# Kernel tuning notes

Hardware: AMD Instinct MI355X
Metric: run time of the kernel (lower is better)

## Reference

```python
import jax, jax.numpy as jnp
import numpy as np

MEM_SIZE = 2000
FEA_DIM = 256
FMAP = 32
BATCH = 32
SHRINK = 0.0025
EPS = 1e-12


def setup_inputs() -> dict:
    key = jax.random.key(0)
    k1, k2, k3, k4 = jax.random.split(key, 4)
    stdv = 1.0 / np.sqrt(FEA_DIM)
    inp = {
        "input": jax.random.normal(k1, (BATCH, FEA_DIM, FMAP, FMAP), dtype=jnp.float32),
        "label_batch": jax.random.randint(k2, (BATCH,), 0, 2),
        "weight": jax.random.uniform(k3, (MEM_SIZE, FEA_DIM), dtype=jnp.float32, minval=-stdv, maxval=stdv),
        "pos_embedding": jax.random.normal(k4, (1, FEA_DIM, FMAP, FMAP), dtype=jnp.float32),
    }
    return inp


def _forward(x, weight, pos_embedding):
    b, c, h, w = x.shape
    m = weight.shape[0]
    x = x + pos_embedding  # pos=True
    xr = x.transpose(0, 2, 3, 1).reshape(-1, c)  # [b*h*w, c]
    # addressing: linear -> softmax over memory slots
    att = jax.nn.softmax(jnp.einsum('nc,mc->nm', xr, weight), axis=1)  # [N, m]
    # compact loss: MSE to nearest memory item (argmax of att before shrink)
    idx = jnp.argmax(att, axis=1)
    pos_item = weight[idx]  # [N, c]
    compact_loss = jnp.mean((xr - pos_item) ** 2)
    # distance loss: hinge on pairwise squared distances between memory items
    sq = jnp.sum(weight * weight, axis=1)
    d2 = sq[:, None] + sq[None, :] - 2.0 * (weight @ weight.T)  # [m, m]
    dist = 1.0 - d2
    dist = dist * (dist > 0).astype(dist.dtype)
    dist = jnp.triu(dist, k=1)
    distance_loss = dist.sum() * 2.0 / (m * (m - 1))
    # hard shrink relu + L1 normalize (shrink_thres > 0)
    att = jax.nn.relu(att - SHRINK) * att / (jnp.abs(att - SHRINK) + EPS)
    att = att / jnp.maximum(jnp.sum(jnp.abs(att), axis=1, keepdims=True), EPS)
    # memory read
    out = jnp.einsum('nm,mc->nc', att, weight)
    out = out.reshape(b, h, w, c).transpose(0, 3, 1, 2)
    return out, compact_loss, distance_loss


def reference(input, label_batch, weight, pos_embedding):
    return _forward(input, weight, pos_embedding)
```

## Files before the change

### kernel.cpp

```cpp
#include <hip/hip_runtime.h>
#include <hip/hip_bf16.h>

typedef unsigned char u8;
typedef unsigned short u16;
typedef unsigned int u32;
typedef long long s64;
typedef float f32x4 __attribute__((ext_vector_type(4)));
typedef long long s64x2 __attribute__((ext_vector_type(2)));

#define MEM    2000
#define FEA    256
#define SLSTR  2064
#define OSTR   265
#define XRS    264
#define POOLSZ 66048
#define OUTN   8388608
#define LSC    0.015625f

__device__ __forceinline__ u32 f2e4m3(float x) {
    float ax = fabsf(x);
    u32 s = (__builtin_bit_cast(u32, x) >> 24) & 0x80u;
    if (ax >= 448.f) return s | 0x7e;
    if (ax < 0.015625f) {
        int q = (int)rintf(ax * 512.f);
        return s | (u32)q;
    }
    int e = (int)(__builtin_bit_cast(u32, ax) >> 23) - 127;
    float scale = __builtin_bit_cast(float, (u32)((127 - e + 3) << 23));
    int q = (int)rintf(ax * scale);
    int E = e + 7;
    if (q == 16) { q = 8; E += 1; if (E > 15) return s | 0x7e; }
    return s | (u32)(E << 3) | (u32)(q & 7);
}
__device__ __forceinline__ u32 f2e4m3_fast(float v) {
    u32 u = __builtin_bit_cast(u32, v);
    u += 0x0007FFFFu + ((u >> 20) & 1u);
    int bb = (int)(u >> 20) - 0x3C0;
    return bb < 0 ? 0u : (u32)bb;
}

__global__ __launch_bounds__(256) void prep_kernel(const float* __restrict__ W,
                                                   u8* __restrict__ WTc,
                                                   u8* __restrict__ Wc,
                                                   float* __restrict__ sqv,
                                                   float* __restrict__ loss) {
    const int blk = blockIdx.x, t = threadIdx.x;
    const int m0 = blk * 8;
    {
        const int sl = t >> 5, cl = t & 31;
        const int slot = m0 + sl;
        const int ch0 = cl * 8;
        const float* wr = W + slot * 256 + ch0;
        f32x4 v0 = *(const f32x4*)wr;
        f32x4 v1 = *(const f32x4*)(wr + 4);
        float ss = v0[0]*v0[0] + v0[1]*v0[1] + v0[2]*v0[2] + v0[3]*v0[3]
                 + v1[0]*v1[0] + v1[1]*v1[1] + v1[2]*v1[2] + v1[3]*v1[3];
        ss += __shfl_xor(ss, 1); ss += __shfl_xor(ss, 2); ss += __shfl_xor(ss, 4);
        ss += __shfl_xor(ss, 8); ss += __shfl_xor(ss, 16);
        if (cl == 0) sqv[slot] = ss;
        const int c = slot >> 6, s = slot & 63;
        const int kk = cl >> 2, agp = cl & 3;
        const int kp = kk >> 1, klo = kk & 1;
        u32 lo = 0, hi = 0;
#pragma unroll
        for (int i = 0; i < 4; ++i) {
            lo |= f2e4m3(v0[i] * 16.f) << (i * 8);
            hi |= f2e4m3(v1[i] * 16.f) << (i * 8);
        }
        u8* dst = Wc + c * 16384 + (size_t)((kp * 4 + agp) * 64 + s) * 16 + klo * 8;
        *(u32*)dst = lo;
        *(u32*)(dst + 4) = hi;
    }
    {
        const int ch = t;
        const int chunk = m0 >> 6;
        const int kl0 = m0 & 63;
        const int klo = kl0 >> 5, agp = (kl0 & 31) >> 3;
        u32 lo = 0, hi = 0;
#pragma unroll
        for (int i = 0; i < 8; ++i) {
            u32 bb = f2e4m3(W[(m0 + i) * 256 + ch] * 16.f);
            if (i < 4) lo |= bb << (i * 8); else hi |= bb << ((i - 4) * 8);
        }
        u8* dst = WTc + chunk * 16384 + ch * 64 + agp * 16 + klo * 8;
        *(u32*)dst = lo;
        *(u32*)(dst + 4) = hi;
    }
    if (blk == 0 && t == 0) {
        loss[0] = 0.0f;
        loss[1] = -2000.0f / (2000.0f * 1999.0f);
    }
}

__global__ __attribute__((amdgpu_flat_work_group_size(512, 512), amdgpu_waves_per_eu(4, 4)))
void main_kernel(
        const float* __restrict__ inp, const float* __restrict__ posb,
        const u8* __restrict__ Wc, const u8* __restrict__ WTc,
        const float* __restrict__ sqv, float* __restrict__ out,
        float* __restrict__ loss) {
    __shared__ __align__(16) u8 pool[POOLSZ];
    __shared__ float sPM[4][32];
    __shared__ int   sPI[4][32];
    __shared__ float sPZ[4][32];
    __shared__ float sPD[4][32];
    __shared__ float sSS[8][32];
    __shared__ float sMax[32];
    __shared__ float sThr[32];
    __shared__ float sInv[32];

    const int t = threadIdx.x;
    const int w = t >> 6, lane = t & 63;
    const int ar = lane & 15, ag = lane >> 4;
    const int blk = blockIdx.x, b = blk >> 5, hw0 = (blk & 31) << 5;
    const int prot = ((blk >> 3) & 15) * 2;
    const int q = w & 3, rt = w >> 2;
    const int row_a = rt * 16 + ar;

    {
        const int hw = t & 31, cg = t >> 5;
        const float* ip = inp + (size_t)b * 262144 + hw0 + hw;
        const float* pp = posb + hw0 + hw;
        float ss = 0.f;
        u8* xrow = pool + hw * XRS + cg * 16;
#pragma unroll
        for (int j = 0; j < 8; ++j) {
            const int ch = cg * 16 + 2 * j;
            float v0 = ip[ch * 1024] + pp[ch * 1024];
            float v1 = ip[(ch + 1) * 1024] + pp[(ch + 1) * 1024];
            ss += v0 * v0 + v1 * v1;
            u16 pk2 = (u16)(f2e4m3(v0 * 4.f) | (f2e4m3(v1 * 4.f) << 8));
            *(u16*)(xrow + 2 * j) = pk2;
        }
        ss += __shfl_xor(ss, 32);
        if (lane < 32) sSS[w][lane] = ss;
    }
    __syncthreads();

    s64 xB[8];
#pragma unroll
    for (int kk = 0; kk < 8; ++kk)
        xB[kk] = *(const s64*)(pool + row_a * XRS + kk * 32 + ag * 8);

    const u8* wbase = Wc + ag * 1024 + (q * 16 + ar) * 16;
    const int c31 = (31 - prot) & 31;

    {
        float bm = -3e38f, zz = 0.f;
        int bi = 0x7fffffff;
#pragma unroll 4
        for (int c = 0; c < 32; ++c) {
            const int pc = (c + prot) & 31;
            const u8* p = wbase + pc * 16384;
            s64x2 w0 = *(const s64x2*)(p);
            s64x2 w1 = *(const s64x2*)(p + 4096);
            s64x2 w2 = *(const s64x2*)(p + 8192);
            s64x2 w3 = *(const s64x2*)(p + 12288);
            f32x4 a = {0.f, 0.f, 0.f, 0.f};
            a = __builtin_amdgcn_mfma_f32_16x16x32_fp8_fp8(w0[0], xB[0], a, 0, 0, 0);
            a = __builtin_amdgcn_mfma_f32_16x16x32_fp8_fp8(w0[1], xB[1], a, 0, 0, 0);
            a = __builtin_amdgcn_mfma_f32_16x16x32_fp8_fp8(w1[0], xB[2], a, 0, 0, 0);
            a = __builtin_amdgcn_mfma_f32_16x16x32_fp8_fp8(w1[1], xB[3], a, 0, 0, 0);
            a = __builtin_amdgcn_mfma_f32_16x16x32_fp8_fp8(w2[0], xB[4], a, 0, 0, 0);
            a = __builtin_amdgcn_mfma_f32_16x16x32_fp8_fp8(w2[1], xB[5], a, 0, 0, 0);
            a = __builtin_amdgcn_mfma_f32_16x16x32_fp8_fp8(w3[0], xB[6], a, 0, 0, 0);
            a = __builtin_amdgcn_mfma_f32_16x16x32_fp8_fp8(w3[1], xB[7], a, 0, 0, 0);
            if (c == c31 && q != 0) { a[0] = -3e38f; a[1] = -3e38f; a[2] = -3e38f; a[3] = -3e38f; }
            const int cb = (pc << 6) + q * 16 + ag * 4;
            const float ob = bm;
#pragma unroll
            for (int e = 0; e < 4; ++e) {
                float v = a[e]; int id = cb + e;
                bool g = (v > bm) || (v == bm && id < bi);
                bm = g ? v : bm;
                bi = g ? id : bi;
            }
            zz *= __expf((ob - bm) * LSC);
            zz += __expf((a[0] - bm) * LSC) + __expf((a[1] - bm) * LSC)
                + __expf((a[2] - bm) * LSC) + __expf((a[3] - bm) * LSC);
        }
#pragma unroll
        for (int d = 16; d < 64; d <<= 1) {
            float om = __shfl_xor(bm, d);
            int   oi = __shfl_xor(bi, d);
            float oz = __shfl_xor(zz, d);
            bool g = (om > bm) || (om == bm && oi < bi);
            float nm = g ? om : bm;
            zz = zz * __expf((bm - nm) * LSC) + oz * __expf((om - nm) * LSC);
            bm = nm;
            bi = g ? oi : bi;
        }
        if (lane < 16) {
            sPM[q][rt * 16 + lane] = bm;
            sPI[q][rt * 16 + lane] = bi;
            sPZ[q][rt * 16 + lane] = zz;
        }
    }
    __syncthreads();

    if (t < 32) {
        float M = sPM[0][t]; int I = sPI[0][t];
#pragma unroll
        for (int qq = 1; qq < 4; ++qq) {
            float m2 = sPM[qq][t]; int i2 = sPI[qq][t];
            bool g = (m2 > M) || (m2 == M && i2 < I);
            M = g ? m2 : M; I = g ? i2 : I;
        }
        float Z = 0.f;
#pragma unroll
        for (int qq = 0; qq < 4; ++qq) Z += sPZ[qq][t] * __expf((sPM[qq][t] - M) * LSC);
        sMax[t] = M;
        sThr[t] = 0.0025f * Z;
        float ssq = 0.f;
#pragma unroll
        for (int ww = 0; ww < 8; ++ww) ssq += sSS[ww][t];
        float term = ssq - 2.f * (M * LSC) + sqv[I];
#pragma unroll
        for (int d = 1; d < 32; d <<= 1) term += __shfl_xor(term, d);
        if (t == 0) atomicAdd(loss, term * (1.0f / 8388608.0f));
    }
    __syncthreads();

    {
        const float M = sMax[row_a];
        const float thrv = sThr[row_a];
        const int newoff = (((q * 2 + (ag >> 1)) & 3) << 4) | ((q >> 1) << 3) | ((ag & 1) << 2);
        const int rowbase = row_a * SLSTR + newoff;
        float den = 0.f;
#pragma unroll 4
        for (int c = 0; c < 32; ++c) {
            const int pc = (c + prot) & 31;
            const u8* p = wbase + pc * 16384;
            s64x2 w0 = *(const s64x2*)(p);
            s64x2 w1 = *(const s64x2*)(p + 4096);
            s64x2 w2 = *(const s64x2*)(p + 8192);
            s64x2 w3 = *(const s64x2*)(p + 12288);
            f32x4 a = {0.f, 0.f, 0.f, 0.f};
            a = __builtin_amdgcn_mfma_f32_16x16x32_fp8_fp8(w0[0], xB[0], a, 0, 0, 0);
            a = __builtin_amdgcn_mfma_f32_16x16x32_fp8_fp8(w0[1], xB[1], a, 0, 0, 0);
            a = __builtin_amdgcn_mfma_f32_16x16x32_fp8_fp8(w1[0], xB[2], a, 0, 0, 0);
            a = __builtin_amdgcn_mfma_f32_16x16x32_fp8_fp8(w1[1], xB[3], a, 0, 0, 0);
            a = __builtin_amdgcn_mfma_f32_16x16x32_fp8_fp8(w2[0], xB[4], a, 0, 0, 0);
            a = __builtin_amdgcn_mfma_f32_16x16x32_fp8_fp8(w2[1], xB[5], a, 0, 0, 0);
            a = __builtin_amdgcn_mfma_f32_16x16x32_fp8_fp8(w3[0], xB[6], a, 0, 0, 0);
            a = __builtin_amdgcn_mfma_f32_16x16x32_fp8_fp8(w3[1], xB[7], a, 0, 0, 0);
            if (c == c31 && q != 0) { a[0] = -3e38f; a[1] = -3e38f; a[2] = -3e38f; a[3] = -3e38f; }
            float a0 = __expf((a[0] - M) * LSC);
            float a1 = __expf((a[1] - M) * LSC);
            float a2 = __expf((a[2] - M) * LSC);
            float a3 = __expf((a[3] - M) * LSC);
            bool k0 = a0 > thrv, k1 = a1 > thrv, k2 = a2 > thrv, k3 = a3 > thrv;
            den += (k0 ? a0 : 0.f) + (k1 ? a1 : 0.f) + (k2 ? a2 : 0.f) + (k3 ? a3 : 0.f);
            u32 pk = (k0 ? f2e4m3_fast(a0 * 64.f) : 0u)
                   | ((k1 ? f2e4m3_fast(a1 * 64.f) : 0u) << 8)
                   | ((k2 ? f2e4m3_fast(a2 * 64.f) : 0u) << 16)
                   | ((k3 ? f2e4m3_fast(a3 * 64.f) : 0u) << 24);
            *(u32*)(pool + rowbase + (pc << 6)) = pk;
        }
        den += __shfl_xor(den, 16);
        den += __shfl_xor(den, 32);
        if (lane < 16) sPD[q][rt * 16 + lane] = den;
    }
    __syncthreads();
    if (t < 32) {
        float dd = sPD[0][t] + sPD[1][t] + sPD[2][t] + sPD[3][t];
        sInv[t] = dd > 0.f ? 1.0f / (1024.0f * dd) : 0.0f;
    }
    __syncthreads();

    const int ch0 = (w * 2) * 16 + ar;
    const int ch1 = ch0 + 16;
    const u8* sLr0 = pool + ar * SLSTR + ag * 16;
    const u8* sLr1 = pool + (16 + ar) * SLSTR + ag * 16;
    const u8* wt0 = WTc + ch0 * 64 + ag * 16;
    const u8* wt1 = WTc + ch1 * 64 + ag * 16;
    f32x4 o00 = {0.f,0.f,0.f,0.f}, o01 = {0.f,0.f,0.f,0.f};
    f32x4 o10 = {0.f,0.f,0.f,0.f}, o11 = {0.f,0.f,0.f,0.f};
#pragma unroll 4
    for (int c = 0; c < 32; ++c) {
        const int pc = (c + prot) & 31;
        const int cc64 = pc << 6;
        s64x2 B0 = *(const s64x2*)(wt0 + pc * 16384);
        s64x2 B1 = *(const s64x2*)(wt1 + pc * 16384);
        s64x2 A0 = *(const s64x2*)(sLr0 + cc64);
        s64x2 A1 = *(const s64x2*)(sLr1 + cc64);
        o00 = __builtin_amdgcn_mfma_f32_16x16x32_fp8_fp8(A0[0], B0[0], o00, 0, 0, 0);
        o00 = __builtin_amdgcn_mfma_f32_16x16x32_fp8_fp8(A0[1], B0[1], o00, 0, 0, 0);
        o01 = __builtin_amdgcn_mfma_f32_16x16x32_fp8_fp8(A1[0], B0[0], o01, 0, 0, 0);
        o01 = __builtin_amdgcn_mfma_f32_16x16x32_fp8_fp8(A1[1], B0[1], o01, 0, 0, 0);
        o10 = __builtin_amdgcn_mfma_f32_16x16x32_fp8_fp8(A0[0], B1[0], o10, 0, 0, 0);
        o10 = __builtin_amdgcn_mfma_f32_16x16x32_fp8_fp8(A0[1], B1[1], o10, 0, 0, 0);
        o11 = __builtin_amdgcn_mfma_f32_16x16x32_fp8_fp8(A1[0], B1[0], o11, 0, 0, 0);
        o11 = __builtin_amdgcn_mfma_f32_16x16x32_fp8_fp8(A1[1], B1[1], o11, 0, 0, 0);
    }
    __syncthreads();

    {
        float* sO = (float*)pool;
#pragma unroll
        for (int i = 0; i < 4; ++i) {
            int r0 = ag * 4 + i, r1 = 16 + ag * 4 + i;
            sO[r0 * OSTR + ch0] = o00[i] * sInv[r0];
            sO[r1 * OSTR + ch0] = o01[i] * sInv[r1];
            sO[r0 * OSTR + ch1] = o10[i] * sInv[r0];
            sO[r1 * OSTR + ch1] = o11[i] * sInv[r1];
        }
    }
    __syncthreads();
    {
        const float* sO = (const float*)pool;
        const int hw = t & 31, cq = t >> 5;
        float* op = out + (size_t)b * 262144 + hw0 + hw;
#pragma unroll
        for (int i = 0; i < 16; ++i) {
            int ch = cq + (i << 4);
            op[ch * 1024] = sO[hw * OSTR + ch];
        }
    }
}

__global__ __launch_bounds__(256) void dist_kernel(const u8* __restrict__ Wc,
                                                   const float* __restrict__ sqv,
                                                   float* __restrict__ dl) {
    __shared__ float red[4];
    int t = threadIdx.x, w = t >> 6, lane = t & 63;
    int ar = lane & 15, ag = lane >> 4;
    const int i0 = blockIdx.x << 4;
    const int ci = i0 >> 6, si0 = i0 & 63;
    s64x2 af2[4];
#pragma unroll
    for (int kp = 0; kp < 4; ++kp)
        af2[kp] = *(const s64x2*)(Wc + ci * 16384 + (size_t)((kp * 4 + ag) * 64 + si0 + ar) * 16);
    float sqi[4];
#pragma unroll
    for (int e = 0; e < 4; ++e) sqi[e] = sqv[i0 + ag * 4 + e];
    float sum = 0.f;
    for (int jt = w; jt < 125; jt += 4) {
        const int j0 = jt << 4;
        const int cj = j0 >> 6, sj0 = j0 & 63;
        f32x4 acc = {0.f, 0.f, 0.f, 0.f};
#pragma unroll
        for (int kp = 0; kp < 4; ++kp) {
            s64x2 bf = *(const s64x2*)(Wc + cj * 16384 + (size_t)((kp * 4 + ag) * 64 + sj0 + ar) * 16);
            acc = __builtin_amdgcn_mfma_f32_16x16x32_fp8_fp8(af2[kp][0], bf[0], acc, 0, 0, 0);
            acc = __builtin_amdgcn_mfma_f32_16x16x32_fp8_fp8(af2[kp][1], bf[1], acc, 0, 0, 0);
        }
        float sqj = sqv[j0 + ar];
#pragma unroll
        for (int e = 0; e < 4; ++e) {
            float dist = 1.0f - (sqi[e] + sqj - acc[e] * 0.0078125f);
            sum += dist > 0.f ? dist : 0.f;
        }
    }
#pragma unroll
    for (int d = 1; d < 64; d <<= 1) sum += __shfl_xor(sum, d);
    if (lane == 0) red[w] = sum;
    __syncthreads();
    if (t == 0) {
        float s = red[0] + red[1] + red[2] + red[3];
        atomicAdd(dl, s * (1.0f / (2000.0f * 1999.0f)));
    }
}

extern "C" void kernel_launch(void* const* d_in, const int* in_sizes, int n_in,
                              void* d_out, int out_size, void* d_ws, size_t ws_size,
                              hipStream_t stream) {
    (void)in_sizes; (void)n_in; (void)out_size; (void)ws_size;
    const float* inp  = (const float*)d_in[0];
    const float* W    = (const float*)d_in[2];
    const float* posb = (const float*)d_in[3];
    float* out = (float*)d_out;

    u8* WTc = (u8*)d_ws;
    u8* Wc  = (u8*)d_ws + 524288;
    float* sqv = (float*)((u8*)d_ws + 1048576);

    hipLaunchKernelGGL(prep_kernel, dim3(250), dim3(256), 0, stream, W, WTc, Wc, sqv, out + OUTN);
    hipLaunchKernelGGL(main_kernel, dim3(1024), dim3(512), 0, stream, inp, posb, Wc, WTc, sqv, out, out + OUTN);
    hipLaunchKernelGGL(dist_kernel, dim3(125), dim3(256), 0, stream, Wc, sqv, out + OUTN + 1);
}
```

Before: 148.2 us.

## Drop online max rescaling in softmax, use unshifted exp2 and hardware fp8 packing

The first pass now sums exp2 of the unshifted scaled logits, which removes the running-max rescale exps and their merges in the shuffle and cross-wave reductions. The second pass thresholds the unshifted exponentials and folds the max shift into a per-row scale and the final normalizer. It also replaces the software fp8 conversion with v_cvt_pk_fp8_f32 and removes the per-block chunk rotation. This cuts transcendental and integer work per element, but risks overflow because logits are not shifted before exponentiation, and dropping the rotation may increase L2 contention on the shared weight chunks.

```diff
diff --git a/kernel.cpp b/kernel.cpp
--- a/kernel.cpp
+++ b/kernel.cpp
@@ -15,7 +15,7 @@
 #define XRS    264
 #define POOLSZ 66048
 #define OUTN   8388608
-#define LSC    0.015625f
+#define LSC2   0.022542108517490387f
 
 __device__ __forceinline__ u32 f2e4m3(float x) {
     float ax = fabsf(x);
@@ -31,12 +31,6 @@
     int E = e + 7;
     if (q == 16) { q = 8; E += 1; if (E > 15) return s | 0x7e; }
     return s | (u32)(E << 3) | (u32)(q & 7);
-}
-__device__ __forceinline__ u32 f2e4m3_fast(float v) {
-    u32 u = __builtin_bit_cast(u32, v);
-    u += 0x0007FFFFu + ((u >> 20) & 1u);
-    int bb = (int)(u >> 20) - 0x3C0;
-    return bb < 0 ? 0u : (u32)bb;
 }
 
 __global__ __launch_bounds__(256) void prep_kernel(const float* __restrict__ W,
@@ -106,13 +100,13 @@
     __shared__ float sSS[8][32];
     __shared__ float sMax[32];
     __shared__ float sThr[32];
+    __shared__ float sSrw[32];
     __shared__ float sInv[32];
 
     const int t = threadIdx.x;
     const int w = t >> 6, lane = t & 63;
     const int ar = lane & 15, ag = lane >> 4;
     const int blk = blockIdx.x, b = blk >> 5, hw0 = (blk & 31) << 5;
-    const int prot = ((blk >> 3) & 15) * 2;
     const int q = w & 3, rt = w >> 2;
     const int row_a = rt * 16 + ar;
 
@@ -142,15 +136,13 @@
         xB[kk] = *(const s64*)(pool + row_a * XRS + kk * 32 + ag * 8);
 
     const u8* wbase = Wc + ag * 1024 + (q * 16 + ar) * 16;
-    const int c31 = (31 - prot) & 31;
-
-    {
-        float bm = -3e38f, zz = 0.f;
+
+    {
+        float bm = -3e38f, z0 = 0.f;
         int bi = 0x7fffffff;
 #pragma unroll 4
         for (int c = 0; c < 32; ++c) {
-            const int pc = (c + prot) & 31;
-            const u8* p = wbase + pc * 16384;
+            const u8* p = wbase + c * 16384;
             s64x2 w0 = *(const s64x2*)(p);
             s64x2 w1 = *(const s64x2*)(p + 4096);
             s64x2 w2 = *(const s64x2*)(p + 8192);
@@ -164,9 +156,8 @@
             a = __builtin_amdgcn_mfma_f32_16x16x32_fp8_fp8(w2[1], xB[5], a, 0, 0, 0);
             a = __builtin_amdgcn_mfma_f32_16x16x32_fp8_fp8(w3[0], xB[6], a, 0, 0, 0);
             a = __builtin_amdgcn_mfma_f32_16x16x32_fp8_fp8(w3[1], xB[7], a, 0, 0, 0);
-            if (c == c31 && q != 0) { a[0] = -3e38f; a[1] = -3e38f; a[2] = -3e38f; a[3] = -3e38f; }
-            const int cb = (pc << 6) + q * 16 + ag * 4;
-            const float ob = bm;
+            if (c == 31 && q != 0) { a[0] = -3e38f; a[1] = -3e38f; a[2] = -3e38f; a[3] = -3e38f; }
+            const int cb = (c << 6) + q * 16 + ag * 4;
 #pragma unroll
             for (int e = 0; e < 4; ++e) {
                 float v = a[e]; int id = cb + e;
@@ -174,25 +165,23 @@
                 bm = g ? v : bm;
                 bi = g ? id : bi;
             }
-            zz *= __expf((ob - bm) * LSC);
-            zz += __expf((a[0] - bm) * LSC) + __expf((a[1] - bm) * LSC)
-                + __expf((a[2] - bm) * LSC) + __expf((a[3] - bm) * LSC);
+            z0 += exp2f(a[0] * LSC2) + exp2f(a[1] * LSC2)
+                + exp2f(a[2] * LSC2) + exp2f(a[3] * LSC2);
         }
 #pragma unroll
         for (int d = 16; d < 64; d <<= 1) {
             float om = __shfl_xor(bm, d);
             int   oi = __shfl_xor(bi, d);
-            float oz = __shfl_xor(zz, d);
+            float oz = __shfl_xor(z0, d);
             bool g = (om > bm) || (om == bm && oi < bi);
-            float nm = g ? om : bm;
-            zz = zz * __expf((bm - nm) * LSC) + oz * __expf((om - nm) * LSC);
-            bm = nm;
+            bm = g ? om : bm;
             bi = g ? oi : bi;
+            z0 += oz;
         }
         if (lane < 16) {
             sPM[q][rt * 16 + lane] = bm;
             sPI[q][rt * 16 + lane] = bi;
-            sPZ[q][rt * 16 + lane] = zz;
+            sPZ[q][rt * 16 + lane] = z0;
         }
     }
     __syncthreads();
@@ -205,15 +194,14 @@
             bool g = (m2 > M) || (m2 == M && i2 < I);
             M = g ? m2 : M; I = g ? i2 : I;
         }
-        float Z = 0.f;
-#pragma unroll
-        for (int qq = 0; qq < 4; ++qq) Z += sPZ[qq][t] * __expf((sPM[qq][t] - M) * LSC);
+        float z0t = sPZ[0][t] + sPZ[1][t] + sPZ[2][t] + sPZ[3][t];
         sMax[t] = M;
-        sThr[t] = 0.0025f * Z;
+        sThr[t] = 0.0025f * z0t;
+        sSrw[t] = 64.f * exp2f(-M * LSC2);
         float ssq = 0.f;
 #pragma unroll
         for (int ww = 0; ww < 8; ++ww) ssq += sSS[ww][t];
-        float term = ssq - 2.f * (M * LSC) + sqv[I];
+        float term = ssq - 2.f * (M * (1.0f / 64.0f)) + sqv[I];
 #pragma unroll
         for (int d = 1; d < 32; d <<= 1) term += __shfl_xor(term, d);
         if (t == 0) atomicAdd(loss, term * (1.0f / 8388608.0f));
@@ -221,15 +209,14 @@
     __syncthreads();
 
     {
-        const float M = sMax[row_a];
-        const float thrv = sThr[row_a];
+        const float thr0 = sThr[row_a];
+        const float Srw  = sSrw[row_a];
         const int newoff = (((q * 2 + (ag >> 1)) & 3) << 4) | ((q >> 1) << 3) | ((ag & 1) << 2);
         const int rowbase = row_a * SLSTR + newoff;
-        float den = 0.f;
+        float denS = 0.f;
 #pragma unroll 4
         for (int c = 0; c < 32; ++c) {
-            const int pc = (c + prot) & 31;
-            const u8* p = wbase + pc * 16384;
+            const u8* p = wbase + c * 16384;
             s64x2 w0 = *(const s64x2*)(p);
             s64x2 w1 = *(const s64x2*)(p + 4096);
             s64x2 w2 = *(const s64x2*)(p + 8192);
@@ -243,27 +230,30 @@
             a = __builtin_amdgcn_mfma_f32_16x16x32_fp8_fp8(w2[1], xB[5], a, 0, 0, 0);
             a = __builtin_amdgcn_mfma_f32_16x16x32_fp8_fp8(w3[0], xB[6], a, 0, 0, 0);
             a = __builtin_amdgcn_mfma_f32_16x16x32_fp8_fp8(w3[1], xB[7], a, 0, 0, 0);
-            if (c == c31 && q != 0) { a[0] = -3e38f; a[1] = -3e38f; a[2] = -3e38f; a[3] = -3e38f; }
-            float a0 = __expf((a[0] - M) * LSC);
-            float a1 = __expf((a[1] - M) * LSC);
-            float a2 = __expf((a[2] - M) * LSC);
-            float a3 = __expf((a[3] - M) * LSC);
-            bool k0 = a0 > thrv, k1 = a1 > thrv, k2 = a2 > thrv, k3 = a3 > thrv;
-            den += (k0 ? a0 : 0.f) + (k1 ? a1 : 0.f) + (k2 ? a2 : 0.f) + (k3 ? a3 : 0.f);
-            u32 pk = (k0 ? f2e4m3_fast(a0 * 64.f) : 0u)
-                   | ((k1 ? f2e4m3_fast(a1 * 64.f) : 0u) << 8)
-                   | ((k2 ? f2e4m3_fast(a2 * 64.f) : 0u) << 16)
-                   | ((k3 ? f2e4m3_fast(a3 * 64.f) : 0u) << 24);
-            *(u32*)(pool + rowbase + (pc << 6)) = pk;
-        }
-        den += __shfl_xor(den, 16);
-        den += __shfl_xor(den, 32);
-        if (lane < 16) sPD[q][rt * 16 + lane] = den;
+            if (c == 31 && q != 0) { a[0] = -3e38f; a[1] = -3e38f; a[2] = -3e38f; a[3] = -3e38f; }
+            float e0 = exp2f(a[0] * LSC2);
+            float e1 = exp2f(a[1] * LSC2);
+            float e2 = exp2f(a[2] * LSC2);
+            float e3 = exp2f(a[3] * LSC2);
+            float v0 = e0 > thr0 ? e0 : 0.f;
+            float v1 = e1 > thr0 ? e1 : 0.f;
+            float v2 = e2 > thr0 ? e2 : 0.f;
+            float v3 = e3 > thr0 ? e3 : 0.f;
+            denS += v0 + v1 + v2 + v3;
+            float f0 = v0 * Srw, f1 = v1 * Srw, f2 = v2 * Srw, f3 = v3 * Srw;
+            u32 pk;
+            asm("v_cvt_pk_fp8_f32 %0, %1, %2" : "=v"(pk) : "v"(f0), "v"(f1));
+            asm("v_cvt_pk_fp8_f32 %0, %1, %2 op_sel:[0,0,1]" : "+v"(pk) : "v"(f2), "v"(f3));
+            *(u32*)(pool + rowbase + (c << 6)) = pk;
+        }
+        denS += __shfl_xor(denS, 16);
+        denS += __shfl_xor(denS, 32);
+        if (lane < 16) sPD[q][rt * 16 + lane] = denS;
     }
     __syncthreads();
     if (t < 32) {
         float dd = sPD[0][t] + sPD[1][t] + sPD[2][t] + sPD[3][t];
-        sInv[t] = dd > 0.f ? 1.0f / (1024.0f * dd) : 0.0f;
+        sInv[t] = dd > 0.f ? exp2f(sMax[t] * LSC2) * (1.0f / 1024.0f) / dd : 0.0f;
     }
     __syncthreads();
 
@@ -277,12 +267,10 @@
     f32x4 o10 = {0.f,0.f,0.f,0.f}, o11 = {0.f,0.f,0.f,0.f};
 #pragma unroll 4
     for (int c = 0; c < 32; ++c) {
-        const int pc = (c + prot) & 31;
-        const int cc64 = pc << 6;
-        s64x2 B0 = *(const s64x2*)(wt0 + pc * 16384);
-        s64x2 B1 = *(const s64x2*)(wt1 + pc * 16384);
-        s64x2 A0 = *(const s64x2*)(sLr0 + cc64);
-        s64x2 A1 = *(const s64x2*)(sLr1 + cc64);
+        s64x2 B0 = *(const s64x2*)(wt0 + c * 16384);
+        s64x2 B1 = *(const s64x2*)(wt1 + c * 16384);
+        s64x2 A0 = *(const s64x2*)(sLr0 + c * 64);
+        s64x2 A1 = *(const s64x2*)(sLr1 + c * 64);
         o00 = __builtin_amdgcn_mfma_f32_16x16x32_fp8_fp8(A0[0], B0[0], o00, 0, 0, 0);
         o00 = __builtin_amdgcn_mfma_f32_16x16x32_fp8_fp8(A0[1], B0[1], o00, 0, 0, 0);
         o01 = __builtin_amdgcn_mfma_f32_16x16x32_fp8_fp8(A1[0], B0[0], o01, 0, 0, 0);
```

Result: slower. 152.6 us (+3.0%).
